# Performance work log

Measured on AMD Instinct MI355X. Metric: run time of the kernel, lower is better.

Reference implementation:

```python
import jax, jax.numpy as jnp
import numpy as np

D_MODEL = 1024
NUM_HEADS = 16
D_K = D_MODEL // NUM_HEADS
R = 8
ALPHA = 16
SCALING = ALPHA / R


def _lora_linear(x, W, b, A, Bm):
    # base: x @ W.T + b ; lora: (x @ A.T) @ Bm.T * scaling
    base = jnp.einsum('btd,od->bto', x, W) + b
    lora = jnp.einsum('btr,or->bto', jnp.einsum('btd,rd->btr', x, A), Bm) * SCALING
    return base + lora


def setup_inputs() -> dict:
    key = jax.random.key(0)
    ks = jax.random.split(key, 20)
    B, T = 2, 2048
    inp = {
        'q': jax.random.normal(ks[0], (B, T, D_MODEL), jnp.float32),
        'k': jax.random.normal(ks[1], (B, T, D_MODEL), jnp.float32),
        'v': jax.random.normal(ks[2], (B, T, D_MODEL), jnp.float32),
        'mask': jnp.ones((1, 1, T, T), jnp.int32),
    }
    i = 3
    for name in ('q', 'k', 'v'):
        inp[f'W{name}'] = jax.random.normal(ks[i], (D_MODEL, D_MODEL), jnp.float32) * 0.02; i += 1
        inp[f'b{name}'] = jnp.zeros((D_MODEL,), jnp.float32)
        inp[f'A{name}'] = jax.random.normal(ks[i], (R, D_MODEL), jnp.float32) * 0.01; i += 1
        inp[f'B{name}'] = jax.random.normal(ks[i], (D_MODEL, R), jnp.float32) * 0.01; i += 1
    inp['Wo'] = jax.random.normal(ks[i], (D_MODEL, D_MODEL), jnp.float32) * 0.02
    inp['bo'] = jnp.zeros((D_MODEL,), jnp.float32)
    return inp


def reference(q, k, v, mask, Wq, bq, Aq, Bq, Wk, bk, Ak, Bk, Wv, bv, Av, Bv, Wo, bo):
    B, Tq, _ = q.shape
    Tk = k.shape[1]
    Q = _lora_linear(q, Wq, bq, Aq, Bq).reshape(B, Tq, NUM_HEADS, D_K).transpose(0, 2, 1, 3)
    K = _lora_linear(k, Wk, bk, Ak, Bk).reshape(B, Tk, NUM_HEADS, D_K).transpose(0, 2, 1, 3)
    V = _lora_linear(v, Wv, bv, Av, Bv).reshape(B, Tk, NUM_HEADS, D_K).transpose(0, 2, 1, 3)
    scores = jnp.einsum('bhqd,bhkd->bhqk', Q, K) / jnp.sqrt(jnp.float32(D_K))
    scores = jnp.where(mask == 0, jnp.float32(-1e9), scores)
    attn = jax.nn.softmax(scores, axis=-1)
    out = jnp.einsum('bhqk,bhkd->bhqd', attn, V)
    out = out.transpose(0, 2, 1, 3).reshape(B, Tq, D_MODEL)
    return jnp.einsum('btd,od->bto', out, Wo) + bo
```

## Files before the change

kernel.cpp:

```cpp
#include <hip/hip_runtime.h>
#include <stdint.h>

typedef unsigned short u16;
typedef __attribute__((ext_vector_type(4))) float f32x4;
typedef __attribute__((ext_vector_type(4))) uint32_t u32x4;
typedef __attribute__((ext_vector_type(8))) __bf16 bf16x8;

#if __has_builtin(__builtin_amdgcn_exp2f)
#define EXP2(x) __builtin_amdgcn_exp2f(x)
#else
#define EXP2(x) exp2f(x)
#endif

static __device__ __forceinline__ float bf2f(u16 u) {
    union { uint32_t i; float f; } v; v.i = ((uint32_t)u) << 16; return v.f;
}
static __device__ __forceinline__ u16 f2bf(float f) {
    union { float f; uint32_t i; } v; v.f = f;
    return (u16)((v.i + 0x7FFFu + ((v.i >> 16) & 1u)) >> 16);
}
static __device__ __forceinline__ uint32_t cvtpk(float lo, float hi) {
    uint32_t r;
    asm("v_cvt_pk_bf16_f32 %0, %1, %2" : "=v"(r) : "v"(lo), "v"(hi));
    return r;
}

static __device__ __forceinline__ void gl2lds16(const u16* g, u16* lds) {
    __builtin_amdgcn_global_load_lds(
        (const __attribute__((address_space(1))) void*)g,
        (__attribute__((address_space(3))) void*)lds, 16, 0, 0);
}

struct CastArgs { const float* src[4]; u16* dst[4]; };

__global__ __launch_bounds__(256)
void cast_kernel(CastArgs a) {
    int bid = blockIdx.x;
    int arr = bid >> 6, boff = bid & 63;
    const float* s = a.src[arr] + (size_t)boff * 16384;
    u16* d = a.dst[arr] + (size_t)boff * 16384;
    const int tid = threadIdx.x;
#pragma unroll
    for (int i = 0; i < 8; ++i) {
        int c = tid + i * 256;
        float4 f0 = *(const float4*)(s + c * 8);
        float4 f1 = *(const float4*)(s + c * 8 + 4);
        u16 o[8];
        o[0] = f2bf(f0.x); o[1] = f2bf(f0.y); o[2] = f2bf(f0.z); o[3] = f2bf(f0.w);
        o[4] = f2bf(f1.x); o[5] = f2bf(f1.y); o[6] = f2bf(f1.z); o[7] = f2bf(f1.w);
        *(uint4*)(d + c * 8) = *(const uint4*)o;
    }
}

__global__ __launch_bounds__(256)
void flags_kernel(const int* __restrict__ mask, int* __restrict__ flags) {
    const int qb = blockIdx.x, kt = blockIdx.y;
    const int tid = threadIdx.x;
    int ok = 1;
#pragma unroll
    for (int i = 0; i < 8; ++i) {
        int c = tid + i * 256;
        int row = c >> 4, cg = c & 15;
        int4 m4 = *(const int4*)&mask[(size_t)(qb * 128 + row) * 2048 + kt * 64 + cg * 4];
        ok &= (m4.x != 0) & (m4.y != 0) & (m4.z != 0) & (m4.w != 0);
    }
    int wall = __all(ok) ? 1 : 0;
    __shared__ int red[4];
    if ((tid & 63) == 0) red[tid >> 6] = wall;
    __syncthreads();
    if (tid == 0) flags[qb * 32 + kt] = red[0] & red[1] & red[2] & red[3];
}

struct XaArgs { const float* x[3]; const float* A[3]; float* o[3]; u16* xb[3]; };

__global__ __launch_bounds__(256)
void xa_kernel(XaArgs a) {
    const int z = blockIdx.y;
    const int row = blockIdx.x * 4 + (threadIdx.x >> 6);
    const int lane = threadIdx.x & 63;
    const float* xr = a.x[z] + (size_t)row * 1024 + lane * 16;
    float xv[16];
#pragma unroll
    for (int j = 0; j < 4; ++j) *(float4*)&xv[j * 4] = *(const float4*)(xr + j * 4);
    {
        u16 ob[16];
#pragma unroll
        for (int j = 0; j < 16; ++j) ob[j] = f2bf(xv[j]);
        u16* dp = a.xb[z] + (size_t)row * 1024 + lane * 16;
        *(uint4*)dp = *(const uint4*)&ob[0];
        *(uint4*)(dp + 8) = *(const uint4*)&ob[8];
    }
    float s[8];
#pragma unroll
    for (int r = 0; r < 8; ++r) {
        const float* ar = a.A[z] + (size_t)r * 1024 + lane * 16;
        float av[16];
#pragma unroll
        for (int j = 0; j < 4; ++j) *(float4*)&av[j * 4] = *(const float4*)(ar + j * 4);
        float acc = 0.f;
#pragma unroll
        for (int j = 0; j < 16; ++j) acc += xv[j] * av[j];
#pragma unroll
        for (int off = 1; off < 64; off <<= 1) acc += __shfl_xor(acc, off, 64);
        s[r] = acc;
    }
    if (lane == 0) {
#pragma unroll
        for (int r = 0; r < 8; ++r) a.o[z][(size_t)row * 8 + r] = s[r];
    }
}

struct GemmPtrs { const u16* X; const u16* W; const float* bias; const float* XA; const float* Bm; void* out; int transT; float oscale; };
struct GemmArgs { GemmPtrs p[3]; };

#define LST 136
#define LTT 72

template <int WMT, int WNT, int LORA>
__global__ __launch_bounds__(256, 2)
void gemm_kernel(GemmArgs args) {
    constexpr int BM = WMT * 32, BN = WNT * 32;
    constexpr int MBLK = 4096 / BM;
    constexpr int IPA = BM / 32;
    constexpr int IPB = BN / 32;
    __shared__ alignas(16) u16 smem[(BM + BN) * 64];
    u16* As = smem;
    u16* Bs = smem + BM * 64;

    const GemmPtrs gp = args.p[blockIdx.z];
    const int tid = threadIdx.x;
    const int lane = tid & 63, wave = tid >> 6;
    const int wm = wave >> 1, wn = wave & 1;
    const int l15 = lane & 15, l4 = lane >> 4;
    const int id = blockIdx.x;
    const int m0 = (id % MBLK) * BM, n0 = (id / MBLK) * BN;

    const int srow = lane >> 3;
    const int scol = ((lane & 7) ^ srow) * 8;
    const u16* gA[IPA];
    const u16* gB[IPB];
#pragma unroll
    for (int i = 0; i < IPA; ++i) {
        int q = wave * IPA + i;
        gA[i] = gp.X + (size_t)(m0 + q * 8 + srow) * 1024 + scol;
    }
#pragma unroll
    for (int i = 0; i < IPB; ++i) {
        int q = wave * IPB + i;
        gB[i] = gp.W + (size_t)(n0 + q * 8 + srow) * 1024 + scol;
    }

    const f32x4 fz = {0.f, 0.f, 0.f, 0.f};
    f32x4 acc[WMT][WNT];
#pragma unroll
    for (int i = 0; i < WMT; ++i)
#pragma unroll
        for (int j = 0; j < WNT; ++j) acc[i][j] = fz;

    const int sw = l15 & 7;
    for (int kb = 0; kb < 16; ++kb) {
        __syncthreads();
#pragma unroll
        for (int i = 0; i < IPA; ++i)
            gl2lds16(gA[i] + kb * 64, &As[(wave * IPA + i) * 512]);
#pragma unroll
        for (int i = 0; i < IPB; ++i)
            gl2lds16(gB[i] + kb * 64, &Bs[(wave * IPB + i) * 512]);
        __syncthreads();
#pragma unroll
        for (int kk2 = 0; kk2 < 2; ++kk2) {
            bf16x8 af[WMT], bfr[WNT];
#pragma unroll
            for (int mt = 0; mt < WMT; ++mt) {
                int x = wm * (WMT * 16) + mt * 16 + l15;
                af[mt] = *(const bf16x8*)&As[x * 64 + (((kk2 * 4 + l4) ^ sw) * 8)];
            }
#pragma unroll
            for (int nt = 0; nt < WNT; ++nt) {
                int y = wn * (WNT * 16) + nt * 16 + l15;
                bfr[nt] = *(const bf16x8*)&Bs[y * 64 + (((kk2 * 4 + l4) ^ sw) * 8)];
            }
#pragma unroll
            for (int mt = 0; mt < WMT; ++mt)
#pragma unroll
                for (int nt = 0; nt < WNT; ++nt)
                    acc[mt][nt] = __builtin_amdgcn_mfma_f32_16x16x32_bf16(af[mt], bfr[nt], acc[mt][nt], 0, 0, 0);
        }
    }

    if constexpr (LORA) {
        __syncthreads();
        float* XAs = (float*)smem;
        float* Bms = (float*)(smem + BM * 64);
        {
            int rr = tid >> 1, hf = (tid & 1) * 4;
            *(float4*)&XAs[rr * 8 + hf] = *(const float4*)&gp.XA[(size_t)(m0 + rr) * 8 + hf];
            if (tid < 128) {
                *(float4*)&Bms[tid * 8]     = *(const float4*)&gp.Bm[(size_t)(n0 + tid) * 8];
                *(float4*)&Bms[tid * 8 + 4] = *(const float4*)&gp.Bm[(size_t)(n0 + tid) * 8 + 4];
            }
        }
        __syncthreads();
        const float osc = gp.oscale;
        float bmv[WNT][8], bsv[WNT];
#pragma unroll
        for (int nt = 0; nt < WNT; ++nt) {
            int nloc = wn * 64 + nt * 16 + l15;
            bsv[nt] = gp.bias[n0 + nloc];
#pragma unroll
            for (int q8 = 0; q8 < 8; ++q8) bmv[nt][q8] = Bms[nloc * 8 + q8];
        }
#pragma unroll
        for (int mt = 0; mt < WMT; ++mt)
#pragma unroll
            for (int r = 0; r < 4; ++r) {
                int mloc = wm * 64 + mt * 16 + l4 * 4 + r;
                float xa8[8];
                *(float4*)&xa8[0] = *(const float4*)&XAs[mloc * 8];
                *(float4*)&xa8[4] = *(const float4*)&XAs[mloc * 8 + 4];
#pragma unroll
                for (int nt = 0; nt < WNT; ++nt) {
                    float lora = 0.f;
#pragma unroll
                    for (int q8 = 0; q8 < 8; ++q8) lora += xa8[q8] * bmv[nt][q8];
                    acc[mt][nt][r] = (acc[mt][nt][r] + bsv[nt] + 2.0f * lora) * osc;
                }
            }
        __syncthreads();

        u16* outp = (u16*)gp.out;
        const int bb = m0 >> 11;
        if (gp.transT) {
            u16* Lst = smem;
#pragma unroll
            for (int ch = 0; ch < 2; ++ch) {
#pragma unroll
                for (int mt2 = 0; mt2 < 2; ++mt2) {
                    int mt = ch * 2 + mt2;
#pragma unroll
                    for (int nt = 0; nt < WNT; ++nt)
#pragma unroll
                        for (int r = 0; r < 4; ++r)
                            Lst[(wn * 64 + nt * 16 + l15) * LTT + wm * 32 + mt2 * 16 + l4 * 4 + r] =
                                f2bf(acc[mt][nt][r]);
                }
                __syncthreads();
#pragma unroll
                for (int j = 0; j < 4; ++j) {
                    int w = tid + j * 256;
                    int nl = w >> 3, seg = w & 7;
                    uint4 val = *(const uint4*)&Lst[nl * LTT + seg * 8];
                    int n = n0 + nl, hh = n >> 6, dd = n & 63;
                    int c0 = seg * 8;
                    int gm = m0 + (c0 >> 5) * 64 + ch * 32 + (c0 & 31);
                    int t = gm & 2047;
                    *(uint4*)&outp[(((size_t)(bb * 16 + hh)) * 64 + dd) * 2048 + t] = val;
                }
                __syncthreads();
            }
        } else {
            u16* Ls = smem;
#pragma unroll
            for (int ch = 0; ch < 2; ++ch) {
#pragma unroll
                for (int mt2 = 0; mt2 < 2; ++mt2) {
                    int mt = ch * 2 + mt2;
#pragma unroll
                    for (int nt = 0; nt < WNT; ++nt)
#pragma unroll
                        for (int r = 0; r < 4; ++r)
                            Ls[(wm * 32 + mt2 * 16 + l4 * 4 + r) * LST + wn * 64 + nt * 16 + l15] =
                                f2bf(acc[mt][nt][r]);
                }
                __syncthreads();
#pragma unroll
                for (int j = 0; j < 4; ++j) {
                    int w = tid + j * 256;
                    int lrow = w >> 4, seg = w & 15;
                    uint4 val = *(const uint4*)&Ls[lrow * LST + seg * 8];
                    int gm = m0 + (lrow >> 5) * 64 + ch * 32 + (lrow & 31);
                    int t = gm & 2047;
                    int n = n0 + seg * 8, hh = n >> 6, dd = n & 63;
                    *(uint4*)&outp[(((size_t)(bb * 16 + hh)) * 2048 + t) * 64 + dd] = val;
                }
                __syncthreads();
            }
        }
    } else {
        float* outp = (float*)gp.out;
#pragma unroll
        for (int mt = 0; mt < WMT; ++mt)
#pragma unroll
            for (int r = 0; r < 4; ++r) {
                int m = m0 + wm * (WMT * 16) + mt * 16 + l4 * 4 + r;
#pragma unroll
                for (int nt = 0; nt < WNT; ++nt) {
                    int n = n0 + wn * (WNT * 16) + nt * 16 + l15;
                    outp[(size_t)m * 1024 + n] = acc[mt][nt][r] + gp.bias[n];
                }
            }
    }
}

#define EXP2C (-5.7707801636f)

__global__ __launch_bounds__(256, 4)
void attn_kernel(const u16* __restrict__ QKV, const int* __restrict__ mask,
                 const int* __restrict__ flags, u16* __restrict__ Xo) {
    const int qb = blockIdx.x >> 5;
    const int bh = blockIdx.x & 31;
    const int b = bh >> 4, h = bh & 15;
    const int tid = threadIdx.x;
    const int lane = tid & 63, wave = tid >> 6;
    const int l15 = lane & 15, l4 = lane >> 4;

    __shared__ alignas(16) u16 Ks[2][64 * 64];
    __shared__ alignas(16) u16 Vts[2][64 * 64];

    const size_t plane = (size_t)2 * 16 * 2048 * 64;
    const u16* Qg = QKV + (size_t)(b * 16 + h) * 2048 * 64;
    const u16* Kg = Qg + plane;
    const u16* Vg = Kg + plane;

    const int srow = lane >> 3;
    const int scol = ((lane & 7) ^ srow) * 8;

    const u16* kbase[2];
    const u16* vbase[2];
#pragma unroll
    for (int i = 0; i < 2; ++i) {
        int qq = wave * 2 + i;
        int kc = 16 * (qq & 1) + 8 * (srow >> 2) + 4 * ((qq >> 1) & 1) + (srow & 3) + 32 * (qq >> 2);
        kbase[i] = Kg + (size_t)kc * 64 + scol;
        vbase[i] = Vg + (size_t)(qq * 8 + srow) * 2048 + scol;
    }

    bf16x8 qa[2];
#pragma unroll
    for (int kk2 = 0; kk2 < 2; ++kk2)
        qa[kk2] = *(const bf16x8*)&Qg[(size_t)(qb * 64 + wave * 16 + l15) * 64 + kk2 * 32 + l4 * 8];

    const f32x4 fz = {0.f, 0.f, 0.f, 0.f};
    f32x4 accO[4];
#pragma unroll
    for (int dt = 0; dt < 4; ++dt) accO[dt] = fz;
    float lsum = 0.f;

#pragma unroll
    for (int i = 0; i < 2; ++i) {
        int qq = wave * 2 + i;
        gl2lds16(kbase[i], &Ks[0][qq * 512]);
        gl2lds16(vbase[i], &Vts[0][qq * 512]);
    }
    __syncthreads();

    for (int kt = 0; kt < 32; ++kt) {
        const u16* Kc = &Ks[kt & 1][0];
        const u16* Vc = &Vts[kt & 1][0];

        if (kt < 31) {
            u16* Kn = &Ks[(kt + 1) & 1][0];
            u16* Vn = &Vts[(kt + 1) & 1][0];
#pragma unroll
            for (int i = 0; i < 2; ++i) {
                int qq = wave * 2 + i;
                gl2lds16(kbase[i] + (size_t)(kt + 1) * 4096, &Kn[qq * 512]);
                gl2lds16(vbase[i] + (size_t)(kt + 1) * 64, &Vn[qq * 512]);
            }
        }

        f32x4 accS[4];
#pragma unroll
        for (int j = 0; j < 4; ++j) accS[j] = fz;
#pragma unroll
        for (int kk2 = 0; kk2 < 2; ++kk2) {
            bf16x8 kf[4];
#pragma unroll
            for (int j = 0; j < 4; ++j)
                kf[j] = *(const bf16x8*)&Kc[(j * 16 + l15) * 64 + (((kk2 * 4 + l4) ^ (l15 & 7)) * 8)];
#pragma unroll
            for (int j = 0; j < 4; ++j)
                accS[j] = __builtin_amdgcn_mfma_f32_16x16x32_bf16(kf[j], qa[kk2], accS[j], 0, 0, 0);
        }

        if (flags[(qb >> 1) * 32 + kt] == 0) {
            int qrow = qb * 64 + wave * 16 + l15;
#pragma unroll
            for (int j = 0; j < 4; ++j)
#pragma unroll
                for (int r = 0; r < 4; ++r) {
                    int kcol = kt * 64 + 8 * l4 + 4 * (j & 1) + r + 32 * (j >> 1);
                    if (mask[(size_t)qrow * 2048 + kcol] == 0) accS[j][r] = -1e9f;
                }
        }

        float part0 = 0.f, part1 = 0.f;
#pragma unroll
        for (int j = 0; j < 4; ++j)
#pragma unroll
            for (int r = 0; r < 4; ++r) {
                float p = EXP2(accS[j][r] + EXP2C);
                accS[j][r] = p;
                if (j & 1) part1 += p; else part0 += p;
            }
        lsum += part0 + part1;

        u32x4 paw0, paw1;
        paw0[0] = cvtpk(accS[0][0], accS[0][1]); paw0[1] = cvtpk(accS[0][2], accS[0][3]);
        paw0[2] = cvtpk(accS[1][0], accS[1][1]); paw0[3] = cvtpk(accS[1][2], accS[1][3]);
        paw1[0] = cvtpk(accS[2][0], accS[2][1]); paw1[1] = cvtpk(accS[2][2], accS[2][3]);
        paw1[2] = cvtpk(accS[3][0], accS[3][1]); paw1[3] = cvtpk(accS[3][2], accS[3][3]);
        bf16x8 pa[2];
        pa[0] = __builtin_bit_cast(bf16x8, paw0);
        pa[1] = __builtin_bit_cast(bf16x8, paw1);

#pragma unroll
        for (int kk2 = 0; kk2 < 2; ++kk2) {
            bf16x8 vf[4];
#pragma unroll
            for (int dt = 0; dt < 4; ++dt)
                vf[dt] = *(const bf16x8*)&Vc[(dt * 16 + l15) * 64 + (((kk2 * 4 + l4) ^ (l15 & 7)) * 8)];
#pragma unroll
            for (int dt = 0; dt < 4; ++dt)
                accO[dt] = __builtin_amdgcn_mfma_f32_16x16x32_bf16(pa[kk2], vf[dt], accO[dt], 0, 0, 0);
        }

        __syncthreads();
    }

    float tot = lsum;
    tot += __shfl_xor(tot, 16, 64);
    tot += __shfl_xor(tot, 32, 64);
    float inv[4];
#pragma unroll
    for (int r = 0; r < 4; ++r) inv[r] = 1.0f / __shfl(tot, l4 * 4 + r, 64);

    u16* Es = &Ks[0][0];
#pragma unroll
    for (int dt = 0; dt < 4; ++dt)
#pragma unroll
        for (int r = 0; r < 4; ++r) {
            int prow = wave * 16 + l4 * 4 + r;
            Es[prow * 64 + (((dt * 2 + (l15 >> 3)) ^ (prow & 7)) * 8) + (l15 & 7)] =
                f2bf(accO[dt][r] * inv[r]);
        }
    __syncthreads();
#pragma unroll
    for (int j = 0; j < 2; ++j) {
        int w = tid + j * 256;
        int row = w >> 3, seg = w & 7;
        uint4 val = *(const uint4*)&Es[row * 64 + ((seg ^ (row & 7)) * 8)];
        int t = qb * 64 + row;
        *(uint4*)&Xo[((size_t)(b * 2048 + t)) * 1024 + h * 64 + seg * 8] = val;
    }
}

extern "C" void kernel_launch(void* const* d_in, const int* in_sizes, int n_in,
                              void* d_out, int out_size, void* d_ws, size_t ws_size,
                              hipStream_t stream) {
    const float* q    = (const float*)d_in[0];
    const float* k    = (const float*)d_in[1];
    const float* v    = (const float*)d_in[2];
    const int*   mask = (const int*)d_in[3];
    const float* Wq = (const float*)d_in[4];
    const float* bq = (const float*)d_in[5];
    const float* Aq = (const float*)d_in[6];
    const float* Bq = (const float*)d_in[7];
    const float* Wk = (const float*)d_in[8];
    const float* bk = (const float*)d_in[9];
    const float* Ak = (const float*)d_in[10];
    const float* Bk = (const float*)d_in[11];
    const float* Wv = (const float*)d_in[12];
    const float* bv = (const float*)d_in[13];
    const float* Av = (const float*)d_in[14];
    const float* Bv = (const float*)d_in[15];
    const float* Wo = (const float*)d_in[16];
    const float* bo = (const float*)d_in[17];

    char* ws = (char*)d_ws;
    u16*   QKV   = (u16*)ws;
    u16*   qb16  = (u16*)(ws + 25165824);
    u16*   kb16  = (u16*)(ws + 33554432);
    u16*   vb16  = (u16*)(ws + 41943040);
    u16*   Wqb   = (u16*)(ws + 50331648);
    u16*   Wkb   = (u16*)(ws + 52428800);
    u16*   Wvb   = (u16*)(ws + 54525952);
    u16*   Wob   = (u16*)(ws + 56623104);
    float* XAbuf = (float*)(ws + 58720256);
    int*   flags = (int*)(ws + 59113472);
    u16*   Xbuf  = qb16;

    flags_kernel<<<dim3(16, 32), dim3(256), 0, stream>>>(mask, flags);

    XaArgs xa;
    xa.x[0] = q;  xa.x[1] = k;  xa.x[2] = v;
    xa.A[0] = Aq; xa.A[1] = Ak; xa.A[2] = Av;
    xa.o[0] = XAbuf; xa.o[1] = XAbuf + 32768; xa.o[2] = XAbuf + 65536;
    xa.xb[0] = qb16; xa.xb[1] = kb16; xa.xb[2] = vb16;
    xa_kernel<<<dim3(1024, 3), dim3(256), 0, stream>>>(xa);

    CastArgs ca;
    ca.src[0] = Wq; ca.src[1] = Wk; ca.src[2] = Wv; ca.src[3] = Wo;
    ca.dst[0] = Wqb; ca.dst[1] = Wkb; ca.dst[2] = Wvb; ca.dst[3] = Wob;
    cast_kernel<<<dim3(256), dim3(256), 0, stream>>>(ca);

    const float QSCALE = 0.1803368801f;
    GemmArgs g1;
    g1.p[0] = GemmPtrs{qb16, Wqb, bq, XAbuf,         Bq, (void*)QKV,             0, QSCALE};
    g1.p[1] = GemmPtrs{kb16, Wkb, bk, XAbuf + 32768, Bk, (void*)(QKV + 4194304), 0, 1.0f};
    g1.p[2] = GemmPtrs{vb16, Wvb, bv, XAbuf + 65536, Bv, (void*)(QKV + 8388608), 1, 1.0f};
    gemm_kernel<4, 4, 1><<<dim3(256, 1, 3), dim3(256), 0, stream>>>(g1);

    attn_kernel<<<dim3(1024), dim3(256), 0, stream>>>(QKV, mask, flags, Xbuf);

    GemmArgs g2;
    g2.p[0] = GemmPtrs{Xbuf, Wob, bo, nullptr, nullptr, d_out, 0, 1.0f};
    g2.p[1] = g2.p[0];
    g2.p[2] = g2.p[0];
    gemm_kernel<2, 4, 0><<<dim3(512, 1, 1), dim3(256), 0, stream>>>(g2);
}
```

Before: 276.3 us.

## Give each attention wave two query tiles to reuse K/V fragments

Shrinks the attention block from four waves to two, so each wave handles 32 query rows (two 16-row tiles) instead of 16. Each K and V fragment read from LDS now feeds two MFMAs, which halves LDS read traffic per unit of compute. Each thread issues twice as many async global-to-LDS copies. The cost is higher register pressure from doubled accumulators, and fewer waves per block for hiding latency, with launch bounds changed to match.

New measurement: 290.0 us. 4.9% more time.

```diff
diff --git a/kernel.cpp b/kernel.cpp
--- a/kernel.cpp
+++ b/kernel.cpp
@@ -304,7 +304,7 @@
 
 #define EXP2C (-5.7707801636f)
 
-__global__ __launch_bounds__(256, 4)
+__global__ __launch_bounds__(128, 2)
 void attn_kernel(const u16* __restrict__ QKV, const int* __restrict__ mask,
                  const int* __restrict__ flags, u16* __restrict__ Xo) {
     const int qb = blockIdx.x >> 5;
@@ -325,30 +325,34 @@
     const int srow = lane >> 3;
     const int scol = ((lane & 7) ^ srow) * 8;
 
-    const u16* kbase[2];
-    const u16* vbase[2];
-#pragma unroll
-    for (int i = 0; i < 2; ++i) {
-        int qq = wave * 2 + i;
+    const u16* kbase[4];
+    const u16* vbase[4];
+#pragma unroll
+    for (int i = 0; i < 4; ++i) {
+        int qq = wave * 4 + i;
         int kc = 16 * (qq & 1) + 8 * (srow >> 2) + 4 * ((qq >> 1) & 1) + (srow & 3) + 32 * (qq >> 2);
         kbase[i] = Kg + (size_t)kc * 64 + scol;
         vbase[i] = Vg + (size_t)(qq * 8 + srow) * 2048 + scol;
     }
 
-    bf16x8 qa[2];
-#pragma unroll
-    for (int kk2 = 0; kk2 < 2; ++kk2)
-        qa[kk2] = *(const bf16x8*)&Qg[(size_t)(qb * 64 + wave * 16 + l15) * 64 + kk2 * 32 + l4 * 8];
+    bf16x8 qa[2][2];
+#pragma unroll
+    for (int qt = 0; qt < 2; ++qt)
+#pragma unroll
+        for (int kk2 = 0; kk2 < 2; ++kk2)
+            qa[qt][kk2] = *(const bf16x8*)&Qg[(size_t)(qb * 64 + wave * 32 + qt * 16 + l15) * 64 + kk2 * 32 + l4 * 8];
 
     const f32x4 fz = {0.f, 0.f, 0.f, 0.f};
-    f32x4 accO[4];
-#pragma unroll
-    for (int dt = 0; dt < 4; ++dt) accO[dt] = fz;
-    float lsum = 0.f;
-
-#pragma unroll
-    for (int i = 0; i < 2; ++i) {
-        int qq = wave * 2 + i;
+    f32x4 accO[2][4];
+#pragma unroll
+    for (int qt = 0; qt < 2; ++qt)
+#pragma unroll
+        for (int dt = 0; dt < 4; ++dt) accO[qt][dt] = fz;
+    float lsum[2] = {0.f, 0.f};
+
+#pragma unroll
+    for (int i = 0; i < 4; ++i) {
+        int qq = wave * 4 + i;
         gl2lds16(kbase[i], &Ks[0][qq * 512]);
         gl2lds16(vbase[i], &Vts[0][qq * 512]);
     }
@@ -362,16 +366,18 @@
             u16* Kn = &Ks[(kt + 1) & 1][0];
             u16* Vn = &Vts[(kt + 1) & 1][0];
 #pragma unroll
-            for (int i = 0; i < 2; ++i) {
-                int qq = wave * 2 + i;
+            for (int i = 0; i < 4; ++i) {
+                int qq = wave * 4 + i;
                 gl2lds16(kbase[i] + (size_t)(kt + 1) * 4096, &Kn[qq * 512]);
                 gl2lds16(vbase[i] + (size_t)(kt + 1) * 64, &Vn[qq * 512]);
             }
         }
 
-        f32x4 accS[4];
-#pragma unroll
-        for (int j = 0; j < 4; ++j) accS[j] = fz;
+        f32x4 accS[2][4];
+#pragma unroll
+        for (int qt = 0; qt < 2; ++qt)
+#pragma unroll
+            for (int j = 0; j < 4; ++j) accS[qt][j] = fz;
 #pragma unroll
         for (int kk2 = 0; kk2 < 2; ++kk2) {
             bf16x8 kf[4];
@@ -379,40 +385,47 @@
             for (int j = 0; j < 4; ++j)
                 kf[j] = *(const bf16x8*)&Kc[(j * 16 + l15) * 64 + (((kk2 * 4 + l4) ^ (l15 & 7)) * 8)];
 #pragma unroll
+            for (int j = 0; j < 4; ++j) {
+                accS[0][j] = __builtin_amdgcn_mfma_f32_16x16x32_bf16(kf[j], qa[0][kk2], accS[0][j], 0, 0, 0);
+                accS[1][j] = __builtin_amdgcn_mfma_f32_16x16x32_bf16(kf[j], qa[1][kk2], accS[1][j], 0, 0, 0);
+            }
+        }
+
+        if (flags[(qb >> 1) * 32 + kt] == 0) {
+#pragma unroll
+            for (int qt = 0; qt < 2; ++qt) {
+                int qrow = qb * 64 + wave * 32 + qt * 16 + l15;
+#pragma unroll
+                for (int j = 0; j < 4; ++j)
+#pragma unroll
+                    for (int r = 0; r < 4; ++r) {
+                        int kcol = kt * 64 + 8 * l4 + 4 * (j & 1) + r + 32 * (j >> 1);
+                        if (mask[(size_t)qrow * 2048 + kcol] == 0) accS[qt][j][r] = -1e9f;
+                    }
+            }
+        }
+
+        bf16x8 pa[2][2];
+#pragma unroll
+        for (int qt = 0; qt < 2; ++qt) {
+            float part0 = 0.f, part1 = 0.f;
+#pragma unroll
             for (int j = 0; j < 4; ++j)
-                accS[j] = __builtin_amdgcn_mfma_f32_16x16x32_bf16(kf[j], qa[kk2], accS[j], 0, 0, 0);
-        }
-
-        if (flags[(qb >> 1) * 32 + kt] == 0) {
-            int qrow = qb * 64 + wave * 16 + l15;
-#pragma unroll
-            for (int j = 0; j < 4; ++j)
 #pragma unroll
                 for (int r = 0; r < 4; ++r) {
-                    int kcol = kt * 64 + 8 * l4 + 4 * (j & 1) + r + 32 * (j >> 1);
-                    if (mask[(size_t)qrow * 2048 + kcol] == 0) accS[j][r] = -1e9f;
-                }
-        }
-
-        float part0 = 0.f, part1 = 0.f;
-#pragma unroll
-        for (int j = 0; j < 4; ++j)
-#pragma unroll
-            for (int r = 0; r < 4; ++r) {
-                float p = EXP2(accS[j][r] + EXP2C);
-                accS[j][r] = p;
-                if (j & 1) part1 += p; else part0 += p;
-            }
-        lsum += part0 + part1;
-
-        u32x4 paw0, paw1;
-        paw0[0] = cvtpk(accS[0][0], accS[0][1]); paw0[1] = cvtpk(accS[0][2], accS[0][3]);
-        paw0[2] = cvtpk(accS[1][0], accS[1][1]); paw0[3] = cvtpk(accS[1][2], accS[1][3]);
-        paw1[0] = cvtpk(accS[2][0], accS[2][1]); paw1[1] = cvtpk(accS[2][2], accS[2][3]);
-        paw1[2] = cvtpk(accS[3][0], accS[3][1]); paw1[3] = cvtpk(accS[3][2], accS[3][3]);
-        bf16x8 pa[2];
-        pa[0] = __builtin_bit_cast(bf16x8, paw0);
-        pa[1] = __builtin_bit_cast(bf16x8, paw1);
+                    float p = EXP2(accS[qt][j][r] + EXP2C);
+                    accS[qt][j][r] = p;
+                    if (j & 1) part1 += p; else part0 += p;
+                }
+            lsum[qt] += part0 + part1;
+            u32x4 paw0, paw1;
+            paw0[0] = cvtpk(accS[qt][0][0], accS[qt][0][1]); paw0[1] = cvtpk(accS[qt][0][2], accS[qt][0][3]);
+            paw0[2] = cvtpk(accS[qt][1][0], accS[qt][1][1]); paw0[3] = cvtpk(accS[qt][1][2], accS[qt][1][3]);
+            paw1[0] = cvtpk(accS[qt][2][0], accS[qt][2][1]); paw1[1] = cvtpk(accS[qt][2][2], accS[qt][2][3]);
+            paw1[2] = cvtpk(accS[qt][3][0], accS[qt][3][1]); paw1[3] = cvtpk(accS[qt][3][2], accS[qt][3][3]);
+            pa[qt][0] = __builtin_bit_cast(bf16x8, paw0);
+            pa[qt][1] = __builtin_bit_cast(bf16x8, paw1);
+        }
 
 #pragma unroll
         for (int kk2 = 0; kk2 < 2; ++kk2) {
@@ -421,33 +434,40 @@
             for (int dt = 0; dt < 4; ++dt)
                 vf[dt] = *(const bf16x8*)&Vc[(dt * 16 + l15) * 64 + (((kk2 * 4 + l4) ^ (l15 & 7)) * 8)];
 #pragma unroll
-            for (int dt = 0; dt < 4; ++dt)
-                accO[dt] = __builtin_amdgcn_mfma_f32_16x16x32_bf16(pa[kk2], vf[dt], accO[dt], 0, 0, 0);
+            for (int dt = 0; dt < 4; ++dt) {
+                accO[0][dt] = __builtin_amdgcn_mfma_f32_16x16x32_bf16(pa[0][kk2], vf[dt], accO[0][dt], 0, 0, 0);
+                accO[1][dt] = __builtin_amdgcn_mfma_f32_16x16x32_bf16(pa[1][kk2], vf[dt], accO[1][dt], 0, 0, 0);
+            }
         }
 
         __syncthreads();
     }
 
-    float tot = lsum;
-    tot += __shfl_xor(tot, 16, 64);
-    tot += __shfl_xor(tot, 32, 64);
-    float inv[4];
-#pragma unroll
-    for (int r = 0; r < 4; ++r) inv[r] = 1.0f / __shfl(tot, l4 * 4 + r, 64);
+    float inv[2][4];
+#pragma unroll
+    for (int qt = 0; qt < 2; ++qt) {
+        float tot = lsum[qt];
+        tot += __shfl_xor(tot, 16, 64);
+        tot += __shfl_xor(tot, 32, 64);
+#pragma unroll
+        for (int r = 0; r < 4; ++r) inv[qt][r] = 1.0f / __shfl(tot, l4 * 4 + r, 64);
+    }
 
     u16* Es = &Ks[0][0];
 #pragma unroll
-    for (int dt = 0; dt < 4; ++dt)
-#pragma unroll
-        for (int r = 0; r < 4; ++r) {
-            int prow = wave * 16 + l4 * 4 + r;
-            Es[prow * 64 + (((dt * 2 + (l15 >> 3)) ^ (prow & 7)) * 8) + (l15 & 7)] =
-                f2bf(accO[dt][r] * inv[r]);
-        }
+    for (int qt = 0; qt < 2; ++qt)
+#pragma unroll
+        for (int dt = 0; dt < 4; ++dt)
+#pragma unroll
+            for (int r = 0; r < 4; ++r) {
+                int prow = wave * 32 + qt * 16 + l4 * 4 + r;
+                Es[prow * 64 + (((dt * 2 + (l15 >> 3)) ^ (prow & 7)) * 8) + (l15 & 7)] =
+                    f2bf(accO[qt][dt][r] * inv[qt][r]);
+            }
     __syncthreads();
 #pragma unroll
-    for (int j = 0; j < 2; ++j) {
-        int w = tid + j * 256;
+    for (int j = 0; j < 4; ++j) {
+        int w = tid + j * 128;
         int row = w >> 3, seg = w & 7;
         uint4 val = *(const uint4*)&Es[row * 64 + ((seg ^ (row & 7)) * 8)];
         int t = qb * 64 + row;
@@ -511,7 +531,7 @@
     g1.p[2] = GemmPtrs{vb16, Wvb, bv, XAbuf + 65536, Bv, (void*)(QKV + 8388608), 1, 1.0f};
     gemm_kernel<4, 4, 1><<<dim3(256, 1, 3), dim3(256), 0, stream>>>(g1);
 
-    attn_kernel<<<dim3(1024), dim3(256), 0, stream>>>(QKV, mask, flags, Xbuf);
+    attn_kernel<<<dim3(1024), dim3(128), 0, stream>>>(QKV, mask, flags, Xbuf);
 
     GemmArgs g2;
     g2.p[0] = GemmPtrs{Xbuf, Wob, bo, nullptr, nullptr, d_out, 0, 1.0f};
```
